# Kernel tuning notes

Measured on AMD Instinct MI355X. Metric: run time of the kernel, lower is better.

## Reference

```python
import jax, jax.numpy as jnp
import numpy as np
from jax import lax

LP, LQ, B, IN = 512, 256, 32, 512
H = 150  # hidden_size*2 hardcoded in module


def setup_inputs() -> dict:
    key = jax.random.key(0)
    ks = jax.random.split(key, 12)
    s = 0.05  # keep tanh/sigmoid unsaturated
    return {
        "up": jax.random.normal(ks[0], (LP, B, IN), jnp.float32),
        "uq": jax.random.normal(ks[1], (LQ, B, IN), jnp.float32),
        "v0": jax.random.normal(ks[2], (B, H), jnp.float32),
        "V": jax.random.normal(ks[3], (B, H), jnp.float32),
        "Wp": jax.random.normal(ks[4], (H, 2 * IN), jnp.float32) * s,
        "Wq": jax.random.normal(ks[5], (H, 2 * IN), jnp.float32) * s,
        "Wv": jax.random.normal(ks[6], (H, H), jnp.float32) * s,
        "Wg": jax.random.normal(ks[7], (4 * IN, 4 * IN), jnp.float32) * s,
        "W_ih": jax.random.normal(ks[8], (3 * H, 2 * IN), jnp.float32) * s,
        "W_hh": jax.random.normal(ks[9], (3 * H, H), jnp.float32) * s,
        "b_ih": jax.random.normal(ks[10], (3 * H,), jnp.float32) * s,
        "b_hh": jax.random.normal(ks[11], (3 * H,), jnp.float32) * s,
    }


def reference(up, uq, v0, V, Wp, Wq, Wv, Wg, W_ih, W_hh, b_ih, b_hh):
    in2 = up.shape[2] * 2
    Up = jnp.concatenate([up, up], axis=2)          # [lp, B, 2*in]
    Uq = jnp.concatenate([uq, uq], axis=2)          # [lq, B, 2*in]
    WqUq = jnp.einsum("qbi,hi->qbh", Uq, Wq)        # hoisted: constant over steps

    def step(v, Up_i):
        Wup = Up_i @ Wp.T                            # [B, H]
        x = jnp.tanh(Wup + WqUq + v @ Wv.T)          # [lq, B, H]
        s = jnp.einsum("qbh,bh->bq", x, V)           # attention logits [B, lq]
        a = jax.nn.softmax(s, axis=1)
        c = jnp.einsum("bq,qbi->bi", a, Uq)          # context [B, 2*in]
        r = jnp.concatenate([Up_i, c], axis=1)       # [B, 4*in]
        g = jax.nn.sigmoid(r @ Wg.T)
        r = g * r
        c_ = r[:, in2:]                              # gated context [B, 2*in]
        # GRUCell
        gi = c_ @ W_ih.T + b_ih
        gh = v @ W_hh.T + b_hh
        i_r, i_z, i_n = jnp.split(gi, 3, axis=1)
        h_r, h_z, h_n = jnp.split(gh, 3, axis=1)
        rg = jax.nn.sigmoid(i_r + h_r)
        zg = jax.nn.sigmoid(i_z + h_z)
        ng = jnp.tanh(i_n + rg * h_n)
        v_new = (1.0 - zg) * ng + zg * v
        return v_new, v_new

    _, vs = lax.scan(step, v0, Up)                   # vs: [lp, B, H]
    return vs  # dropout = identity (eval)
```

## Files before the change

kernel.cpp:

```cpp
#include <hip/hip_runtime.h>
#include <hip/hip_bf16.h>

#define AGENT __HIP_MEMORY_SCOPE_AGENT
#define RLX __ATOMIC_RELAXED
typedef unsigned long long u64t;

typedef _Float16 h2 __attribute__((ext_vector_type(2)));
union U32H2 { unsigned u; h2 h; };
__device__ __forceinline__ h2 uh(unsigned u){ U32H2 c; c.u=u; return c.h; }
__device__ __forceinline__ unsigned pk(float a, float b){
  U32H2 c; c.h = h2{(_Float16)a, (_Float16)b}; return c.u;
}
#define RCPF(x) __builtin_amdgcn_rcpf(x)

__device__ __forceinline__ float DOT2(unsigned a, unsigned b, float acc){
#if __has_builtin(__builtin_amdgcn_fdot2)
  return __builtin_amdgcn_fdot2(uh(a), uh(b), acc, false);
#else
  h2 x = uh(a), y = uh(b);
  acc = fmaf((float)x[0], (float)y[0], acc);
  return fmaf((float)x[1], (float)y[1], acc);
#endif
}
__device__ __forceinline__ float sigm(float x){ return RCPF(1.0f+__expf(-x)); }
__device__ __forceinline__ float ftanh(float x){ return 1.0f - 2.0f*RCPF(1.0f+__expf(x+x)); }

__device__ __forceinline__ void pubw(u64t* p, unsigned seq, unsigned data){
  __hip_atomic_store(p, ((u64t)seq<<32)|(u64t)data, RLX, AGENT);
}
template<int K>
__device__ __forceinline__ void waitN(const u64t* base, const int* off, unsigned seq,
                                      unsigned* out, unsigned* kf){
  long n=0;
  for(;;){
    u64t v[K]; bool ok=true;
    #pragma unroll
    for(int k=0;k<K;k++) v[k]=__hip_atomic_load(base+off[k], RLX, AGENT);
    #pragma unroll
    for(int k=0;k<K;k++) ok &= ((unsigned)(v[k]>>32)==seq);
    if(ok){
      #pragma unroll
      for(int k=0;k<K;k++) out[k]=(unsigned)v[k];
      return;
    }
    __builtin_amdgcn_s_sleep(1);
    if((++n&255)==0){
      if(__hip_atomic_load(kf,RLX,AGENT)!=0u) break;
      if(n>300000L){ __hip_atomic_store(kf,1u,RLX,AGENT); break; }
    }
  }
  #pragma unroll
  for(int k=0;k<K;k++) out[k]=0u;
}

__global__ void k_fold(const float* __restrict__ Wp, const float* __restrict__ Wq,
                       const float* __restrict__ Wg,
                       float* __restrict__ WpT, float* __restrict__ WqT,
                       float* __restrict__ WgupT, float* __restrict__ WgcT)
{
  int i0 = blockIdx.x*blockDim.x+threadIdx.x;
  int st = gridDim.x*blockDim.x;
  for(int o=i0;o<512*150;o+=st){ int h=o%150, i=o/150;
    WpT[o]=Wp[h*1024+i]+Wp[h*1024+512+i];
    WqT[o]=Wq[h*1024+i]+Wq[h*1024+512+i]; }
  for(int o=i0;o<512*1024;o+=st){ int i=o&511, j=o>>9;
    size_t rb=(size_t)(1024+j)*2048;
    WgupT[(size_t)i*1024+j]=Wg[rb+i]+Wg[rb+512+i];
    WgcT [(size_t)i*1024+j]=Wg[rb+1024+i]+Wg[rb+1536+i]; }
}

__global__ void k_fold2(const float* __restrict__ Wih,
                        const float* __restrict__ Whh, const float* __restrict__ Wv,
                        unsigned* __restrict__ WihT,
                        unsigned* __restrict__ WhhP, unsigned* __restrict__ WvU)
{
  int i0 = blockIdx.x*blockDim.x+threadIdx.x;
  int st = gridDim.x*blockDim.x;
  for(int o=i0;o<512*456;o+=st){ int k=o%456, jp=o/456;
    unsigned v = 0u;
    if(k<450) v = pk(Wih[(size_t)k*1024+2*jp], Wih[(size_t)k*1024+2*jp+1]);
    WihT[o] = v; }
  for(int o=i0;o<76*456;o+=st){ int k=o%456, p=o/456;
    float x=0.f,y=0.f;
    if(k<450){ if(2*p<150) x=Whh[k*150+2*p]; if(2*p+1<150) y=Whh[k*150+2*p+1]; }
    WhhP[o]=pk(x,y); }
  for(int o=i0;o<76*152;o+=st){ int h=o%152, p=o/152;
    float x=0.f,y=0.f;
    if(h<150){ if(2*p<150) x=Wv[h*150+2*p]; if(2*p+1<150) y=Wv[h*150+2*p+1]; }
    WvU[o]=pk(x,y); }
}

__global__ __launch_bounds__(256) void k_uqp(const float* __restrict__ uq, unsigned* __restrict__ uqP){
  __shared__ float Al[32*512];
  int b = blockIdx.x, qt = blockIdx.y, tid = threadIdx.x;
  for(int o4=tid;o4<4096;o4+=256){ int m=o4>>7, i4=o4&127;
    ((float4*)Al)[o4] = *(const float4*)&uq[(size_t)(qt*32+m)*16384 + b*512 + i4*4]; }
  __syncthreads();
  for(int o=tid;o<8192;o+=256){ int i=o>>4, p=o&15;
    uqP[((size_t)b*512+i)*128 + qt*16 + p] = pk(Al[(2*p)*512+i], Al[(2*p+1)*512+i]); }
}

template<int MODE>
__global__ __launch_bounds__(256) void k_gemm(const float* __restrict__ A,
   const float* __restrict__ WT, _Float16* __restrict__ oH, int N)
{
  __shared__ float Al[32*512];
  int mt=blockIdx.x, nt=blockIdx.y, tid=threadIdx.x;
  const float* Ab = A + (size_t)mt*16384;
  for(int o=tid;o<4096;o+=256) ((float4*)Al)[o]=((const float4*)Ab)[o];
  __syncthreads();
  int n = nt*256+tid;
  if(n>=N) return;
  float acc[32];
  #pragma unroll
  for(int m=0;m<32;m++) acc[m]=0.f;
  const float* wp = WT + n;
  #pragma unroll 2
  for(int k=0;k<512;k+=2){
    float w0 = wp[(size_t)k*N], w1 = wp[(size_t)(k+1)*N];
    #pragma unroll
    for(int m=0;m<32;m++) acc[m]=fmaf(w0, Al[m*512+k], acc[m]);
    #pragma unroll
    for(int m=0;m<32;m++) acc[m]=fmaf(w1, Al[m*512+k+1], acc[m]);
  }
  if(MODE==0){
    #pragma unroll
    for(int m=0;m<32;m++) oH[((size_t)m*512 + mt)*152 + n] = (_Float16)acc[m];
  } else if(MODE==3){
    #pragma unroll
    for(int m=0;m<32;m++) oH[((size_t)m*256 + mt)*152 + n] = (_Float16)acc[m];
  } else {
    #pragma unroll
    for(int m=0;m<32;m++) oH[((size_t)m*512 + mt)*1024 + n] = (_Float16)acc[m];
  }
}

__global__ __launch_bounds__(256) void k_gemmM(const float* __restrict__ uq,
   const float* __restrict__ WgcT, unsigned* __restrict__ Mp)
{
  __shared__ float Al[32*512];
  int b=blockIdx.x, qt=blockIdx.y, nt=blockIdx.z, tid=threadIdx.x;
  for(int o4=tid;o4<4096;o4+=256){ int m=o4>>7, i4=o4&127;
    ((float4*)Al)[o4] = *(const float4*)&uq[(size_t)(qt*32+m)*16384 + b*512 + i4*4]; }
  __syncthreads();
  int n = nt*256+tid;
  float acc[32];
  #pragma unroll
  for(int m=0;m<32;m++) acc[m]=0.f;
  const float* wp = WgcT + n;
  #pragma unroll 2
  for(int k=0;k<512;k+=2){
    float w0 = wp[(size_t)k*1024], w1 = wp[(size_t)(k+1)*1024];
    #pragma unroll
    for(int m=0;m<32;m++) acc[m]=fmaf(w0, Al[m*512+k], acc[m]);
    #pragma unroll
    for(int m=0;m<32;m++) acc[m]=fmaf(w1, Al[m*512+k+1], acc[m]);
  }
  #pragma unroll
  for(int p=0;p<16;p++)
    Mp[((size_t)b*1024 + n)*128 + qt*16 + p] = pk(acc[2*p], acc[2*p+1]);
}

__global__ void k_init(unsigned* comm){
  int i = blockIdx.x*blockDim.x + threadIdx.x;
  if(i < 66052) comm[i] = 0u;
}

struct __align__(16) SMO {
  unsigned WvU[76*152];
  unsigned WqUq[256*76];
  unsigned wup[80], vp[80];
  float V[152], v[152], w2[152], s[256];
  float gi[452], rgh[2][452], bi[452], bh[452];
};
struct __align__(16) SMW {
  unsigned M[128*265];
  unsigned a2[128], gup[128], cpr[128];
  float ccf[128], Gc[256], rgi[2][452];
};
union SMU { SMO o; SMW w; };

__global__ __launch_bounds__(1024) void persist(
  const unsigned* __restrict__ uqP,   const unsigned* __restrict__ Mp,
  const unsigned* __restrict__ Gup3u, const unsigned* __restrict__ Wuphu,
  const unsigned* __restrict__ WqUqhu, const unsigned* __restrict__ WihTu,
  const unsigned* __restrict__ WhhP,  const unsigned* __restrict__ WvUg,
  const float* __restrict__ v0, const float* __restrict__ Vin,
  const float* __restrict__ bih, const float* __restrict__ bhh,
  u64t* aP, u64t* giP, unsigned* kf,
  float* __restrict__ dout)
{
  extern __shared__ char smraw[];
  SMU& S = *reinterpret_cast<SMU*>(smraw);
  const int tid = threadIdx.x;
  const int bid = blockIdx.x;

  if(bid < 32){
    const int b = bid;
    for(int o=tid;o<11552;o+=1024) S.o.WvU[o]=WvUg[o];
    for(int o=tid;o<19456;o+=1024){ int q=o/76,w=o%76;
      S.o.WqUq[o]=WqUqhu[((size_t)b*256+q)*76+w]; }
    for(int o=tid;o<152;o+=1024){
      S.o.V[o]=(o<150)?Vin[b*150+o]:0.f;
      S.o.v[o]=(o<150)?v0[b*150+o]:0.f; }
    for(int o=tid;o<452;o+=1024){
      S.o.bi[o]=(o<450)?bih[o]:0.f;
      S.o.bh[o]=(o<450)?bhh[o]:0.f; }
    __syncthreads();
    if(tid<76) S.o.vp[tid]=pk(S.o.v[2*tid], S.o.v[2*tid+1]);
    __syncthreads();

    const int gib = b*904;
    for(int t=0;t<512;++t){
      if(tid<76) S.o.wup[tid]=Wuphu[((size_t)b*512+t)*76+tid];
      if(t>0){
        if(tid<225){
          int off[4]={gib+tid, gib+226+tid, gib+452+tid, gib+678+tid};
          unsigned gv[4];
          waitN<4>(giP,off,(unsigned)t,gv,kf);
          float g0=0.f,g1=0.f;
          #pragma unroll
          for(int k=0;k<4;k++){ h2 x=uh(gv[k]); g0+=(float)x[0]; g1+=(float)x[1]; }
          S.o.gi[2*tid]=g0; S.o.gi[2*tid+1]=g1;
        }
        __syncthreads();
        if(tid<75){
          int h0=2*tid, h1=h0+1;
          float gh00=S.o.rgh[0][h0]+S.o.rgh[1][h0]+S.o.bh[h0];
          float gh10=S.o.rgh[0][150+h0]+S.o.rgh[1][150+h0]+S.o.bh[150+h0];
          float gh20=S.o.rgh[0][300+h0]+S.o.rgh[1][300+h0]+S.o.bh[300+h0];
          float rg0=sigm(S.o.gi[h0]+S.o.bi[h0]+gh00);
          float zg0=sigm(S.o.gi[150+h0]+S.o.bi[150+h0]+gh10);
          float ng0=ftanh(S.o.gi[300+h0]+S.o.bi[300+h0]+rg0*gh20);
          float vn0=fmaf(zg0, S.o.v[h0]-ng0, ng0);
          float gh01=S.o.rgh[0][h1]+S.o.rgh[1][h1]+S.o.bh[h1];
          float gh11=S.o.rgh[0][150+h1]+S.o.rgh[1][150+h1]+S.o.bh[150+h1];
          float gh21=S.o.rgh[0][300+h1]+S.o.rgh[1][300+h1]+S.o.bh[300+h1];
          float rg1=sigm(S.o.gi[h1]+S.o.bi[h1]+gh01);
          float zg1=sigm(S.o.gi[150+h1]+S.o.bi[150+h1]+gh11);
          float ng1=ftanh(S.o.gi[300+h1]+S.o.bi[300+h1]+rg1*gh21);
          float vn1=fmaf(zg1, S.o.v[h1]-ng1, ng1);
          S.o.v[h0]=vn0; S.o.v[h1]=vn1;
          S.o.vp[tid]=pk(vn0,vn1);
          dout[((size_t)(t-1)*32+b)*150+h0]=vn0;
          dout[((size_t)(t-1)*32+b)*150+h1]=vn1;
        }
      }
      __syncthreads();
      if(tid<608){
        int h=tid>>2, qd=tid&3;
        float acc=0.f;
        if(h<150){
          #pragma unroll
          for(int p=qd*19;p<qd*19+19;p++) acc=DOT2(S.o.WvU[p*152+h], S.o.vp[p], acc);
        }
        acc+=__shfl_xor(acc,1,64); acc+=__shfl_xor(acc,2,64);
        if(h<150&&qd==0){ h2 ww=uh(S.o.wup[h>>1]); S.o.w2[h]=acc+(float)ww[h&1]; }
      }
      __syncthreads();
      {
        int q=tid>>2, hq=tid&3;
        int hp0=hq*19, hp1=(hq==3)?75:hp0+19;
        float acc=0.f;
        for(int hp=hp0;hp<hp1;hp++){
          h2 wp=uh(S.o.WqUq[q*76+hp]);
          acc=fmaf(S.o.V[2*hp],   ftanh(S.o.w2[2*hp]  +(float)wp[0]), acc);
          acc=fmaf(S.o.V[2*hp+1], ftanh(S.o.w2[2*hp+1]+(float)wp[1]), acc);
        }
        acc+=__shfl_xor(acc,1,64); acc+=__shfl_xor(acc,2,64);
        if(hq==0) S.o.s[q]=acc;
      }
      __syncthreads();
      if(tid<64){
        float x0=S.o.s[tid],x1=S.o.s[tid+64],x2=S.o.s[tid+128],x3=S.o.s[tid+192];
        float mx=fmaxf(fmaxf(x0,x1),fmaxf(x2,x3));
        #pragma unroll
        for(int o=1;o<64;o<<=1) mx=fmaxf(mx,__shfl_xor(mx,o,64));
        float e0=__expf(x0-mx),e1=__expf(x1-mx),e2=__expf(x2-mx),e3=__expf(x3-mx);
        float sm=e0+e1+e2+e3;
        #pragma unroll
        for(int o=1;o<64;o<<=1) sm+=__shfl_xor(sm,o,64);
        float rs=RCPF(sm);
        float a0=e0*rs, a1=e1*rs, a2v=e2*rs, a3=e3*rs;
        float y0=__shfl_xor(a0,1,64), y1=__shfl_xor(a1,1,64);
        float y2=__shfl_xor(a2v,1,64), y3=__shfl_xor(a3,1,64);
        if(!(tid&1)){
          int w=tid>>1;
          pubw(aP+b*128+w,    (unsigned)(t+1), pk(a0,y0));
          pubw(aP+b*128+32+w, (unsigned)(t+1), pk(a1,y1));
          pubw(aP+b*128+64+w, (unsigned)(t+1), pk(a2v,y2));
          pubw(aP+b*128+96+w, (unsigned)(t+1), pk(a3,y3));
        }
      }
      {
        int k=tid&511, half=tid>>9;
        if(k<450){
          float ah=0.f;
          int p0=half*38, p1=half?76:38;
          for(int p=p0;p<p1;p++) ah=DOT2(WhhP[p*456+k], S.o.vp[p], ah);
          S.o.rgh[half][k]=ah;
        }
      }
    }
    if(tid<225){
      int off[4]={gib+tid, gib+226+tid, gib+452+tid, gib+678+tid};
      unsigned gv[4];
      waitN<4>(giP,off,512u,gv,kf);
      float g0=0.f,g1=0.f;
      #pragma unroll
      for(int k=0;k<4;k++){ h2 x=uh(gv[k]); g0+=(float)x[0]; g1+=(float)x[1]; }
      S.o.gi[2*tid]=g0; S.o.gi[2*tid+1]=g1;
    }
    __syncthreads();
    if(tid<150){
      float gh0=S.o.rgh[0][tid]+S.o.rgh[1][tid]+S.o.bh[tid];
      float gh1=S.o.rgh[0][150+tid]+S.o.rgh[1][150+tid]+S.o.bh[150+tid];
      float gh2=S.o.rgh[0][300+tid]+S.o.rgh[1][300+tid]+S.o.bh[300+tid];
      float rg=sigm(S.o.gi[tid]+S.o.bi[tid] + gh0);
      float zg=sigm(S.o.gi[150+tid]+S.o.bi[150+tid] + gh1);
      float ng=ftanh(S.o.gi[300+tid]+S.o.bi[300+tid] + rg*gh2);
      dout[((size_t)511*32+b)*150+tid]=fmaf(zg, S.o.v[tid]-ng, ng);
    }

  } else {
    const int wid = bid-32;
    const int b = wid>>2, s = wid&3;
    for(int o=tid;o<32768;o+=1024){
      int qp=o&127, jl=o>>7;
      int j = s*128 + (jl&127) + ((jl>>7)<<9);
      S.w.M[qp*265+jl] = Mp[((size_t)b*1024+j)*128+qp];
    }
    __syncthreads();
    const size_t uqbase = ((size_t)b*512 + s*128)*128;
    for(int t=0;t<512;++t){
      if(tid<128){
        int wi = (tid<64)? (s*64+tid) : (256+s*64+tid-64);
        unsigned gupr = Gup3u[((size_t)b*512+t)*512 + wi];
        int off[1]={b*128+tid};
        unsigned av[1];
        waitN<1>(aP,off,(unsigned)(t+1),av,kf);
        S.w.a2[tid]=av[0];
        S.w.gup[tid]=gupr;
      }
      __syncthreads();
      {
        int i=tid>>3, q8=tid&7;
        float acc=0.f;
        const unsigned* up = uqP + uqbase + (size_t)i*128;
        #pragma unroll 4
        for(int kk=0;kk<16;kk++){
          int qp=kk*8+q8;
          acc=DOT2(S.w.a2[qp], up[qp], acc);
        }
        acc+=__shfl_xor(acc,1,64); acc+=__shfl_xor(acc,2,64); acc+=__shfl_xor(acc,4,64);
        if(q8==0) S.w.ccf[i]=acc;
      }
      {
        int jl=tid>>2, qc=tid&3;
        float acc=0.f;
        #pragma unroll 8
        for(int kk=0;kk<32;kk++){
          int qp=kk*4+qc;
          acc=DOT2(S.w.a2[qp], S.w.M[qp*265+jl], acc);
        }
        acc+=__shfl_xor(acc,1,64); acc+=__shfl_xor(acc,2,64);
        if(qc==0) S.w.Gc[jl]=acc;
      }
      __syncthreads();
      if(tid<128){
        h2 gv=uh(S.w.gup[tid]);
        float c0=sigm(S.w.Gc[2*tid]  +(float)gv[0])*S.w.ccf[(2*tid)&127];
        float c1=sigm(S.w.Gc[2*tid+1]+(float)gv[1])*S.w.ccf[(2*tid+1)&127];
        S.w.cpr[tid]=pk(c0,c1);
      }
      __syncthreads();
      {
        int k=tid&511, half=tid>>9;
        float acc=0.f;
        if(k<450){
          #pragma unroll 8
          for(int m=0;m<64;m++){
            int jpg = half*256 + s*64 + m;
            acc=DOT2(WihTu[(size_t)jpg*456+k], S.w.cpr[half*64+m], acc);
          }
          S.w.rgi[half][k]=acc;
        }
      }
      __syncthreads();
      if(tid<225){
        float g0=S.w.rgi[0][2*tid]+S.w.rgi[1][2*tid];
        float g1=S.w.rgi[0][2*tid+1]+S.w.rgi[1][2*tid+1];
        pubw(giP + ((size_t)b*4+s)*226 + tid, (unsigned)(t+1), pk(g0,g1));
      }
    }
  }
}

extern "C" void kernel_launch(void* const* d_in, const int* in_sizes, int n_in,
                              void* d_out, int out_size, void* d_ws, size_t ws_size,
                              hipStream_t stream)
{
  const float* up  = (const float*)d_in[0];
  const float* uq  = (const float*)d_in[1];
  const float* v0  = (const float*)d_in[2];
  const float* Vm  = (const float*)d_in[3];
  const float* Wp  = (const float*)d_in[4];
  const float* Wq  = (const float*)d_in[5];
  const float* Wv  = (const float*)d_in[6];
  const float* Wg  = (const float*)d_in[7];
  const float* W_ih= (const float*)d_in[8];
  const float* W_hh= (const float*)d_in[9];
  const float* b_ih= (const float*)d_in[10];
  const float* b_hh= (const float*)d_in[11];
  float* dout = (float*)d_out;
  char* wsb = (char*)d_ws;

  size_t off = 0;
  auto alloc = [&](size_t bytes)->size_t{ size_t p = off; off = (off + bytes + 255) & ~(size_t)255; return p; };
  size_t oWgupT = alloc((size_t)512*1024*4);
  size_t oWgcT  = alloc((size_t)512*1024*4);
  size_t oWuph  = alloc((size_t)32*512*152*2);
  size_t oWqUqh = alloc((size_t)32*256*152*2);
  size_t oWihT  = alloc((size_t)512*456*4);
  size_t oWhhP  = alloc((size_t)76*456*4);
  size_t oWvU   = alloc((size_t)76*152*4);
  size_t oUqP   = alloc((size_t)32*512*128*4);
  size_t oMp    = alloc((size_t)32*1024*128*4);
  size_t oGup3  = alloc((size_t)32*512*1024*2);
  if(ws_size < off) return;

  float*    WgupT = (float*)(wsb + oWgupT);
  float*    WgcT  = (float*)(wsb + oWgcT);
  _Float16* Wuph  = (_Float16*)(wsb + oWuph);
  _Float16* WqUqh = (_Float16*)(wsb + oWqUqh);
  unsigned* WihT  = (unsigned*)(wsb + oWihT);
  unsigned* WhhP  = (unsigned*)(wsb + oWhhP);
  unsigned* WvU   = (unsigned*)(wsb + oWvU);
  unsigned* uqP   = (unsigned*)(wsb + oUqP);
  unsigned* Mp    = (unsigned*)(wsb + oMp);
  _Float16* Gup3  = (_Float16*)(wsb + oGup3);
  float* WpT = (float*)(wsb + oGup3);
  float* WqT = (float*)(wsb + oGup3 + 307456);

  u64t* comm64 = (u64t*)(wsb + oWgupT);
  u64t* aP  = comm64;
  u64t* giP = comm64 + 4096;
  unsigned* kf = (unsigned*)(comm64 + 33024);

  k_fold <<<256,256,0,stream>>>(Wp,Wq,Wg, WpT,WqT,WgupT,WgcT);
  k_fold2<<<256,256,0,stream>>>(W_ih, W_hh, Wv, WihT, WhhP, WvU);
  k_uqp  <<<dim3(32,8),256,0,stream>>>(uq, uqP);
  k_gemm<0><<<dim3(512,1),256,0,stream>>>(up, WpT, Wuph, 150);
  k_gemm<3><<<dim3(256,1),256,0,stream>>>(uq, WqT, WqUqh, 150);
  k_gemm<4><<<dim3(512,4),256,0,stream>>>(up, WgupT, Gup3, 1024);
  k_gemmM<<<dim3(32,8,4),256,0,stream>>>(uq, WgcT, Mp);
  k_init <<<65,1024,0,stream>>>((unsigned*)comm64);

  int smem = (int)sizeof(SMU);
  hipFuncSetAttribute((const void*)persist, hipFuncAttributeMaxDynamicSharedMemorySize, smem);
  const unsigned* Gup3u  = (const unsigned*)Gup3;
  const unsigned* Wuphu  = (const unsigned*)Wuph;
  const unsigned* WqUqhu = (const unsigned*)WqUqh;
  void* ka[16] = { (void*)&uqP, (void*)&Mp, (void*)&Gup3u, (void*)&Wuphu, (void*)&WqUqhu,
                   (void*)&WihT, (void*)&WhhP, (void*)&WvU,
                   (void*)&v0, (void*)&Vm, (void*)&b_ih, (void*)&b_hh,
                   (void*)&aP, (void*)&giP, (void*)&kf, (void*)&dout };
  hipLaunchCooperativeKernel((const void*)persist, dim3(160), dim3(1024), ka,
                             (unsigned)smem, stream);
}
```

Before: 6.873 ms.

## Fold fourth context-gating slice into owner block, drop to 3 workers per batch

The owner block for each batch now computes the fourth quarter of the gated context and its partial W_ih product itself, reading uq and Mp directly from global memory, instead of waiting on a fourth worker block. The grid shrinks from 160 to 128 cooperative blocks and the per-step gi wait covers three published partials rather than four. This cuts one block's cross-block publish and wait per step, but it lengthens the owner's serial per-step critical path with extra global reads and syncs.

```diff
diff --git a/kernel.cpp b/kernel.cpp
--- a/kernel.cpp
+++ b/kernel.cpp
@@ -163,7 +163,7 @@
 
 __global__ void k_init(unsigned* comm){
   int i = blockIdx.x*blockDim.x + threadIdx.x;
-  if(i < 66052) comm[i] = 0u;
+  if(i < 51600) comm[i] = 0u;
 }
 
 struct __align__(16) SMO {
@@ -171,7 +171,9 @@
   unsigned WqUq[256*76];
   unsigned wup[80], vp[80];
   float V[152], v[152], w2[152], s[256];
-  float gi[452], rgh[2][452], bi[452], bh[452];
+  unsigned a2[128], gup[128], cpr[128];
+  float ccf[128], Gc[256];
+  float gi[452], rgh[2][452], rgo[2][452], bi[452], bh[452];
 };
 struct __align__(16) SMW {
   unsigned M[128*265];
@@ -206,21 +208,27 @@
     for(int o=tid;o<452;o+=1024){
       S.o.bi[o]=(o<450)?bih[o]:0.f;
       S.o.bh[o]=(o<450)?bhh[o]:0.f; }
+    for(int o=tid;o<904;o+=1024){ S.o.rgo[o/452][o%452]=0.f; }
     __syncthreads();
     if(tid<76) S.o.vp[tid]=pk(S.o.v[2*tid], S.o.v[2*tid+1]);
     __syncthreads();
 
-    const int gib = b*904;
+    const int gib = b*678;
     for(int t=0;t<512;++t){
       if(tid<76) S.o.wup[tid]=Wuphu[((size_t)b*512+t)*76+tid];
+      if(tid<128){
+        int wi = (tid<64)? (192+tid) : (448+tid-64);
+        S.o.gup[tid] = Gup3u[((size_t)b*512+t)*512 + wi];
+      }
       if(t>0){
         if(tid<225){
-          int off[4]={gib+tid, gib+226+tid, gib+452+tid, gib+678+tid};
-          unsigned gv[4];
-          waitN<4>(giP,off,(unsigned)t,gv,kf);
-          float g0=0.f,g1=0.f;
+          int off[3]={gib+tid, gib+226+tid, gib+452+tid};
+          unsigned gv[3];
+          waitN<3>(giP,off,(unsigned)t,gv,kf);
+          float g0=S.o.rgo[0][2*tid]+S.o.rgo[1][2*tid];
+          float g1=S.o.rgo[0][2*tid+1]+S.o.rgo[1][2*tid+1];
           #pragma unroll
-          for(int k=0;k<4;k++){ h2 x=uh(gv[k]); g0+=(float)x[0]; g1+=(float)x[1]; }
+          for(int k=0;k<3;k++){ h2 x=uh(gv[k]); g0+=(float)x[0]; g1+=(float)x[1]; }
           S.o.gi[2*tid]=g0; S.o.gi[2*tid+1]=g1;
         }
         __syncthreads();
@@ -286,12 +294,61 @@
         float y2=__shfl_xor(a2v,1,64), y3=__shfl_xor(a3,1,64);
         if(!(tid&1)){
           int w=tid>>1;
-          pubw(aP+b*128+w,    (unsigned)(t+1), pk(a0,y0));
-          pubw(aP+b*128+32+w, (unsigned)(t+1), pk(a1,y1));
-          pubw(aP+b*128+64+w, (unsigned)(t+1), pk(a2v,y2));
-          pubw(aP+b*128+96+w, (unsigned)(t+1), pk(a3,y3));
-        }
-      }
+          unsigned p0=pk(a0,y0), p1=pk(a1,y1), p2=pk(a2v,y2), p3=pk(a3,y3);
+          pubw(aP+b*128+w,    (unsigned)(t+1), p0);
+          pubw(aP+b*128+32+w, (unsigned)(t+1), p1);
+          pubw(aP+b*128+64+w, (unsigned)(t+1), p2);
+          pubw(aP+b*128+96+w, (unsigned)(t+1), p3);
+          S.o.a2[w]=p0; S.o.a2[32+w]=p1; S.o.a2[64+w]=p2; S.o.a2[96+w]=p3;
+        }
+      }
+      __syncthreads();
+      {
+        int i=tid>>3, q8=tid&7;
+        float acc=0.f;
+        const unsigned* up = uqP + ((size_t)b*512 + 384 + i)*128;
+        #pragma unroll 4
+        for(int kk=0;kk<16;kk++){
+          int qp=kk*8+q8;
+          acc=DOT2(S.o.a2[qp], up[qp], acc);
+        }
+        acc+=__shfl_xor(acc,1,64); acc+=__shfl_xor(acc,2,64); acc+=__shfl_xor(acc,4,64);
+        if(q8==0) S.o.ccf[i]=acc;
+      }
+      {
+        int jl=tid>>2, qc=tid&3;
+        int j = 384 + (jl&127) + ((jl>>7)<<9);
+        const unsigned* mrow = Mp + ((size_t)b*1024+j)*128;
+        float acc=0.f;
+        #pragma unroll 8
+        for(int kk=0;kk<32;kk++){
+          int qp=kk*4+qc;
+          acc=DOT2(S.o.a2[qp], mrow[qp], acc);
+        }
+        acc+=__shfl_xor(acc,1,64); acc+=__shfl_xor(acc,2,64);
+        if(qc==0) S.o.Gc[jl]=acc;
+      }
+      __syncthreads();
+      if(tid<128){
+        h2 gv=uh(S.o.gup[tid]);
+        float c0=sigm(S.o.Gc[2*tid]  +(float)gv[0])*S.o.ccf[(2*tid)&127];
+        float c1=sigm(S.o.Gc[2*tid+1]+(float)gv[1])*S.o.ccf[(2*tid+1)&127];
+        S.o.cpr[tid]=pk(c0,c1);
+      }
+      __syncthreads();
+      {
+        int k=tid&511, half=tid>>9;
+        float acc=0.f;
+        if(k<450){
+          #pragma unroll 8
+          for(int m=0;m<64;m++){
+            int jpg = half*256 + 192 + m;
+            acc=DOT2(WihTu[(size_t)jpg*456+k], S.o.cpr[half*64+m], acc);
+          }
+          S.o.rgo[half][k]=acc;
+        }
+      }
+      __syncthreads();
       {
         int k=tid&511, half=tid>>9;
         if(k<450){
@@ -303,12 +360,13 @@
       }
     }
     if(tid<225){
-      int off[4]={gib+tid, gib+226+tid, gib+452+tid, gib+678+tid};
-      unsigned gv[4];
-      waitN<4>(giP,off,512u,gv,kf);
-      float g0=0.f,g1=0.f;
+      int off[3]={gib+tid, gib+226+tid, gib+452+tid};
+      unsigned gv[3];
+      waitN<3>(giP,off,512u,gv,kf);
+      float g0=S.o.rgo[0][2*tid]+S.o.rgo[1][2*tid];
+      float g1=S.o.rgo[0][2*tid+1]+S.o.rgo[1][2*tid+1];
       #pragma unroll
-      for(int k=0;k<4;k++){ h2 x=uh(gv[k]); g0+=(float)x[0]; g1+=(float)x[1]; }
+      for(int k=0;k<3;k++){ h2 x=uh(gv[k]); g0+=(float)x[0]; g1+=(float)x[1]; }
       S.o.gi[2*tid]=g0; S.o.gi[2*tid+1]=g1;
     }
     __syncthreads();
@@ -324,7 +382,7 @@
 
   } else {
     const int wid = bid-32;
-    const int b = wid>>2, s = wid&3;
+    const int b = wid/3, s = wid-3*b;
     for(int o=tid;o<32768;o+=1024){
       int qp=o&127, jl=o>>7;
       int j = s*128 + (jl&127) + ((jl>>7)<<9);
@@ -390,7 +448,7 @@
       if(tid<225){
         float g0=S.w.rgi[0][2*tid]+S.w.rgi[1][2*tid];
         float g1=S.w.rgi[0][2*tid+1]+S.w.rgi[1][2*tid+1];
-        pubw(giP + ((size_t)b*4+s)*226 + tid, (unsigned)(t+1), pk(g0,g1));
+        pubw(giP + ((size_t)b*3+s)*226 + tid, (unsigned)(t+1), pk(g0,g1));
       }
     }
   }
@@ -445,7 +503,7 @@
   u64t* comm64 = (u64t*)(wsb + oWgupT);
   u64t* aP  = comm64;
   u64t* giP = comm64 + 4096;
-  unsigned* kf = (unsigned*)(comm64 + 33024);
+  unsigned* kf = (unsigned*)(comm64 + 25792);
 
   k_fold <<<256,256,0,stream>>>(Wp,Wq,Wg, WpT,WqT,WgupT,WgcT);
   k_fold2<<<256,256,0,stream>>>(W_ih, W_hh, Wv, WihT, WhhP, WvU);
@@ -454,7 +512,7 @@
   k_gemm<3><<<dim3(256,1),256,0,stream>>>(uq, WqT, WqUqh, 150);
   k_gemm<4><<<dim3(512,4),256,0,stream>>>(up, WgupT, Gup3, 1024);
   k_gemmM<<<dim3(32,8,4),256,0,stream>>>(uq, WgcT, Mp);
-  k_init <<<65,1024,0,stream>>>((unsigned*)comm64);
+  k_init <<<51,1024,0,stream>>>((unsigned*)comm64);
 
   int smem = (int)sizeof(SMU);
   hipFuncSetAttribute((const void*)persist, hipFuncAttributeMaxDynamicSharedMemorySize, smem);
@@ -465,6 +523,6 @@
                    (void*)&WihT, (void*)&WhhP, (void*)&WvU,
                    (void*)&v0, (void*)&Vm, (void*)&b_ih, (void*)&b_hh,
                    (void*)&aP, (void*)&giP, (void*)&kf, (void*)&dout };
-  hipLaunchCooperativeKernel((const void*)persist, dim3(160), dim3(1024), ka,
+  hipLaunchCooperativeKernel((const void*)persist, dim3(128), dim3(1024), ka,
                              (unsigned)smem, stream);
 }
```

Result: slower. 9.460 ms (+37.6%).
